# Kernel tuning notes

Hardware: AMD Instinct MI355X
Metric: run time of the kernel (lower is better)

Reference implementation:

```python
import math
import jax, jax.numpy as jnp
import numpy as np

B, S, H, NH = 4, 2048, 1024, 16
HD = H // NH  # 64


def _rope_cos_sin(seq_len, dim, base=10000.0):
    # freqs[j] = base^(-2j/dim), angles = outer(t, freqs)
    inv = 1.0 / (base ** (jnp.arange(0, dim, 2, dtype=jnp.float32) / dim))
    t = jnp.arange(seq_len, dtype=jnp.float32)
    ang = jnp.outer(t, inv)  # (S, dim//2)
    return jnp.cos(ang), jnp.sin(ang)


def _apply_rope(x, cos, sin):
    # x: (B, S, NH, HD); pairs are (x[2i], x[2i+1]) per torch view_as_complex on reshape(..., -1, 2)
    xr = x.reshape(*x.shape[:-1], HD // 2, 2)
    x0, x1 = xr[..., 0], xr[..., 1]
    c = cos[None, :, None, :]  # (1, S, 1, HD//2)
    s = sin[None, :, None, :]
    o0 = x0 * c - x1 * s
    o1 = x0 * s + x1 * c
    return jnp.stack([o0, o1], axis=-1).reshape(x.shape)


def setup_inputs() -> dict:
    key = jax.random.key(0)
    ks = jax.random.split(key, 5)
    scale = 1.0 / math.sqrt(H)
    return {
        "x": jax.random.normal(ks[0], (B, S, H), dtype=jnp.float32),
        "wq": jax.random.normal(ks[1], (H, H), dtype=jnp.float32) * scale,
        "wk": jax.random.normal(ks[2], (H, H), dtype=jnp.float32) * scale,
        "wv": jax.random.normal(ks[3], (H, H), dtype=jnp.float32) * scale,
        "wo": jax.random.normal(ks[4], (H, H), dtype=jnp.float32) * scale,
        "attention_mask": jnp.ones((B, S), dtype=jnp.int32),
    }


def reference(x, wq, wk, wv, wo, attention_mask):
    # Linear(bias=False): y = x @ W.T with W shape (out, in)
    q = jnp.einsum('bsh,oh->bso', x, wq).reshape(B, S, NH, HD)
    k = jnp.einsum('bsh,oh->bso', x, wk).reshape(B, S, NH, HD)
    v = jnp.einsum('bsh,oh->bso', x, wv).reshape(B, S, NH, HD)
    cos, sin = _rope_cos_sin(S, HD)
    q = _apply_rope(q, cos, sin)
    k = _apply_rope(k, cos, sin)
    # scores: (B, NH, S, S)
    scores = jnp.einsum('bqhd,bkhd->bhqk', q, k) / math.sqrt(HD)
    mask = attention_mask[:, None, None, :]  # (B,1,1,S)
    scores = jnp.where(mask == 0, -jnp.inf, scores)
    attn = jax.nn.softmax(scores, axis=-1)
    # attn_dropout: eval mode / p=0 -> identity
    out = jnp.einsum('bhqk,bkhd->bqhd', attn, v).reshape(B, S, H)
    return jnp.einsum('bsh,oh->bso', out, wo)
```

## Files before the change

kernel.cpp:

```cpp
#include <hip/hip_runtime.h>
#include <hip/hip_bf16.h>

#define B_   4
#define S_   2048
#define H_   1024
#define NH_  16
#define HD_  64
#define M_   8192
#define K_   1024

using bf16x8 = __bf16 __attribute__((ext_vector_type(8)));
using f32x4  = float __attribute__((ext_vector_type(4)));
using f32x16 = float __attribute__((ext_vector_type(16)));

__device__ inline f32x4 mfma16(bf16x8 a, bf16x8 b, f32x4 c) {
    return __builtin_amdgcn_mfma_f32_16x16x32_bf16(a, b, c, 0, 0, 0);
}
__device__ inline f32x16 mfma32(bf16x8 a, bf16x8 b, f32x16 c) {
    return __builtin_amdgcn_mfma_f32_32x32x16_bf16(a, b, c, 0, 0, 0);
}

__device__ inline unsigned short f2bf(float f) {
    __hip_bfloat16 h = __float2bfloat16(f);
    return *reinterpret_cast<unsigned short*>(&h);
}

__device__ inline unsigned cvt_pk_bf16(float lo, float hi) {
    unsigned r;
    asm("v_cvt_pk_bf16_f32 %0, %1, %2" : "=v"(r) : "v"(lo), "v"(hi));
    return r;
}

__device__ inline void perm32swap(unsigned &a, unsigned &b) {
    asm("v_permlane32_swap_b32 %0, %1" : "+v"(a), "+v"(b));
}

__device__ inline void gload_lds16(const unsigned short* g, unsigned short* l) {
    __builtin_amdgcn_global_load_lds(
        (const __attribute__((address_space(1))) void*)g,
        (__attribute__((address_space(3))) void*)l, 16, 0, 0);
}

#define EXP2F(x) __builtin_amdgcn_exp2f(x)


__global__ __launch_bounds__(256) void prep_convert(
    const float* __restrict__ x,  const float* __restrict__ wq,
    const float* __restrict__ wk, const float* __restrict__ wv,
    const float* __restrict__ wo, unsigned short* __restrict__ ws)
{
    size_t u = (size_t)blockIdx.x * 256 + threadIdx.x;
    const float* src; unsigned short* dst; size_t off;
    if (u < 2097152)      { src = x;  dst = ws;            off = u * 4; }
    else if (u < 2359296) { src = wq; dst = ws + 8388608;  off = (u - 2097152) * 4; }
    else if (u < 2621440) { src = wk; dst = ws + 9437184;  off = (u - 2359296) * 4; }
    else if (u < 2883584) { src = wv; dst = ws + 10485760; off = (u - 2621440) * 4; }
    else                  { src = wo; dst = ws + 11534336; off = (u - 2883584) * 4; }
    float4 v = *reinterpret_cast<const float4*>(src + off);
    ushort4 o;
    o.x = f2bf(v.x); o.y = f2bf(v.y); o.z = f2bf(v.z); o.w = f2bf(v.w);
    *reinterpret_cast<ushort4*>(dst + off) = o;
}

__global__ __launch_bounds__(256) void rope_table(
    float2* __restrict__ ropeb, const int* __restrict__ mask,
    float* __restrict__ biasb, int* __restrict__ kflagb)
{
    int idx = blockIdx.x * 256 + threadIdx.x;
    int pos = idx >> 5, i = idx & 31;
    float inv = expf(-(float)(2 * i) * (9.210340371976184f / 64.0f));
    float ang = (float)pos * inv;
    float2 cs; cs.x = cosf(ang); cs.y = sinf(ang);
    ropeb[idx] = cs;
    if (idx < B_ * S_)
        biasb[idx] = mask[idx] ? 0.0f : -__builtin_inff();
    if (idx < B_ * 32) {
        int b = idx >> 5, kt = idx & 31;
        int all = 1;
        for (int j = 0; j < 64; j++)
            all &= (mask[b * S_ + kt * 64 + j] != 0) ? 1 : 0;
        kflagb[idx] = all;
    }
}

template<int MODE>
__global__ __launch_bounds__(256, 2) void gemm_main(
    const unsigned short* __restrict__ A,
    const unsigned short* __restrict__ W,
    unsigned short* __restrict__ qbuf, unsigned short* __restrict__ kbuf,
    unsigned short* __restrict__ vtb, float* __restrict__ fout,
    const float* __restrict__ ropeb)
{
    __shared__ alignas(16) unsigned short Al[2][128 * 64];
    __shared__ alignas(16) unsigned short Bl[2][128 * 64];

    const int t = threadIdx.x;
    const int l = t & 63;
    const int w = t >> 6;
    const int lane_r = l & 15, lane_g = l >> 4;
    const int bn = blockIdx.x, bm = blockIdx.y;
    const size_t rowbase = (size_t)bm * 128;
    const int colbase = bn * 128;
    const int wm = (w >> 1) * 64, wn = (w & 1) * 64;
    const int which = (MODE == 0) ? (colbase >> 10) : 3;
    const float scale = (which == 0) ? 0.18033688089184827f : 1.0f;

    const int glrow  = l >> 3;
    const int glslot = (l & 7) ^ glrow;
    const unsigned short* ga = A + (rowbase + w * 8 + glrow) * K_ + glslot * 8;
    const unsigned short* gb = W + (size_t)(colbase + w * 8 + glrow) * K_ + glslot * 8;

#define GLA(bi, kt, i) gload_lds16(ga + (size_t)(i) * 32 * K_ + (kt) * 64, \
                                   &Al[bi][((i) * 32 + w * 8) * 64]);
#define GLB(bi, kt, i) gload_lds16(gb + (size_t)(i) * 32 * K_ + (kt) * 64, \
                                   &Bl[bi][((i) * 32 + w * 8) * 64]);
#define RDA(mt, kk) { int rowa = wm + (mt) * 16 + lane_r;                      \
    af[mt][kk] = *reinterpret_cast<const bf16x8*>((const char*)Al[cur] +       \
        ((rowa * 128 + (kk) * 64 + lane_g * 16) ^ ((rowa & 7) << 4))); }
#define RDB(nt, kk) { int rowb = wn + (nt) * 16 + lane_r;                      \
    bfr[nt][kk] = *reinterpret_cast<const bf16x8*>((const char*)Bl[cur] +      \
        ((rowb * 128 + (kk) * 64 + lane_g * 16) ^ ((rowb & 7) << 4))); }
#define MM(mb, nb)                                                             \
    if (MODE == 0 && which <= 1) {                                             \
        _Pragma("unroll")                                                      \
        for (int a = (nb); a < (nb) + 2; a++)                                  \
            _Pragma("unroll")                                                  \
            for (int b2 = (mb); b2 < (mb) + 2; b2++) {                         \
                acc[a][b2] = mfma16(bfr[a][0], af[b2][0], acc[a][b2]);         \
                acc[a][b2] = mfma16(bfr[a][1], af[b2][1], acc[a][b2]);         \
            }                                                                  \
    } else {                                                                   \
        _Pragma("unroll")                                                      \
        for (int mt = (mb); mt < (mb) + 2; mt++)                               \
            _Pragma("unroll")                                                  \
            for (int nt = (nb); nt < (nb) + 2; nt++) {                         \
                acc[mt][nt] = mfma16(af[mt][0], bfr[nt][0], acc[mt][nt]);      \
                acc[mt][nt] = mfma16(af[mt][1], bfr[nt][1], acc[mt][nt]);      \
            }                                                                  \
    }
#define BARS __builtin_amdgcn_s_barrier();                                     \
             asm volatile("s_waitcnt lgkmcnt(0)" ::: "memory");                \
             __builtin_amdgcn_s_setprio(1);
#define BARE __builtin_amdgcn_s_setprio(0); __builtin_amdgcn_s_barrier();

    f32x4 zero4 = {0.f, 0.f, 0.f, 0.f};
    f32x4 acc[4][4];
#pragma unroll
    for (int a = 0; a < 4; a++)
#pragma unroll
        for (int b2 = 0; b2 < 4; b2++) acc[a][b2] = zero4;

    GLA(0, 0, 0) GLA(0, 0, 1) GLA(0, 0, 2) GLA(0, 0, 3)
    GLB(0, 0, 0) GLB(0, 0, 1) GLB(0, 0, 2) GLB(0, 0, 3)
    __syncthreads();

    for (int kt = 0; kt < 16; kt++) {
        const int cur = kt & 1, nxt = cur ^ 1;
        const bool pf = (kt < 15);
        bf16x8 af[4][2], bfr[4][2];
        RDA(0, 0) RDA(0, 1) RDA(1, 0) RDA(1, 1)
        RDB(0, 0) RDB(0, 1) RDB(1, 0) RDB(1, 1)
        if (pf) { GLA(nxt, kt + 1, 0) GLA(nxt, kt + 1, 1) GLA(nxt, kt + 1, 2) }
        BARS MM(0, 0) BARE
        RDB(2, 0) RDB(2, 1) RDB(3, 0) RDB(3, 1)
        if (pf) { GLA(nxt, kt + 1, 3) GLB(nxt, kt + 1, 0) GLB(nxt, kt + 1, 1) }
        BARS MM(0, 2) BARE
        RDA(2, 0) RDA(2, 1) RDA(3, 0) RDA(3, 1)
        if (pf) { GLB(nxt, kt + 1, 2) GLB(nxt, kt + 1, 3) }
        BARS MM(2, 2) BARE
        __builtin_amdgcn_s_setprio(1);
        MM(2, 0)
        __builtin_amdgcn_s_setprio(0);
        asm volatile("s_waitcnt vmcnt(0)" ::: "memory");
        __builtin_amdgcn_s_barrier();
    }
#undef GLA
#undef GLB
#undef RDA
#undef RDB
#undef MM
#undef BARS
#undef BARE

    if (MODE == 1) {
        float* out = fout;
#pragma unroll
        for (int mt = 0; mt < 4; mt++)
#pragma unroll
            for (int nt = 0; nt < 4; nt++)
#pragma unroll
                for (int i = 0; i < 4; i++) {
                    size_t r = rowbase + wm + mt * 16 + lane_g * 4 + i;
                    int n = colbase + wn + nt * 16 + lane_r;
                    out[r * 1024 + n] = acc[mt][nt][i];
                }
    } else if (which <= 1) {
        unsigned short* out = which ? kbuf : qbuf;
#pragma unroll
        for (int a = 0; a < 4; a++) {
            int nbase = (colbase & 1023) + wn + a * 16 + 4 * lane_g;
            int h = nbase >> 6, d0 = nbase & 63;
#pragma unroll
            for (int b2 = 0; b2 < 4; b2++) {
                size_t r = rowbase + wm + b2 * 16 + lane_r;
                int bb  = (int)(r >> 11);
                int pos = (int)(r & 2047);
                float4 cs = *reinterpret_cast<const float4*>(
                    ropeb + pos * 64 + d0);
                float a0 = acc[a][b2][0], a1 = acc[a][b2][1];
                float a2 = acc[a][b2][2], a3 = acc[a][b2][3];
                float o0 = (a0 * cs.x - a1 * cs.y) * scale;
                float o1 = (a0 * cs.y + a1 * cs.x) * scale;
                float o2 = (a2 * cs.z - a3 * cs.w) * scale;
                float o3 = (a2 * cs.w + a3 * cs.z) * scale;
                uint2 o;
                o.x = cvt_pk_bf16(o0, o1);
                o.y = cvt_pk_bf16(o2, o3);
                *reinterpret_cast<uint2*>(
                    out + (((size_t)(bb * NH_ + h)) * S_ + pos) * 64 + d0) = o;
            }
        }
    } else {
#pragma unroll
        for (int a = 0; a < 4; a++)
#pragma unroll
            for (int b2 = 0; b2 < 4; b2++) {
                size_t rr = rowbase + wm + a * 16 + lane_g * 4;
                int n = (colbase & 1023) + wn + b2 * 16 + lane_r;
                int bb  = (int)(rr >> 11);
                int pos = (int)(rr & 2047);
                int h = n >> 6, d = n & 63;
                ushort4 o;
                o.x = f2bf(acc[a][b2][0]); o.y = f2bf(acc[a][b2][1]);
                o.z = f2bf(acc[a][b2][2]); o.w = f2bf(acc[a][b2][3]);
                *reinterpret_cast<ushort4*>(
                    vtb + (((size_t)(bb * NH_ + h)) * 64 + d) * S_ + pos) = o;
            }
    }
}

__global__ __launch_bounds__(256, 2) void attn_fwd(
    const unsigned short* __restrict__ qb, const unsigned short* __restrict__ kb,
    const unsigned short* __restrict__ vt, const float* __restrict__ biasb,
    const int* __restrict__ kflagb, unsigned short* __restrict__ ao)
{
    __shared__ alignas(16) unsigned short Kl[2][64 * 64];
    __shared__ alignas(16) unsigned short Vl[2][64 * 64];

    const int bid = blockIdx.x;
    const int xcd = bid & 7, idx = bid >> 3;
    const int bh = xcd * 8 + (idx >> 3);
    const int qt = idx & 7;
    const int b = bh >> 4, h = bh & 15;

    const int t = threadIdx.x, l = t & 63, w = t >> 6;
    const int lr = l & 31;
    const int hi = l >> 5;
    const int row8 = lr & 7;

    const unsigned short* qp = qb + (size_t)bh * S_ * 64;
    const unsigned short* kp = kb + (size_t)bh * S_ * 64;
    const unsigned short* vp = vt + (size_t)bh * 64 * S_;
    const float* bp = biasb + (size_t)b * S_;
    const int* kfl = kflagb + b * 32;

    bf16x8 qf[2][4];
#pragma unroll
    for (int qbk = 0; qbk < 2; qbk++) {
        int qrow = qt * 256 + w * 64 + qbk * 32 + lr;
#pragma unroll
        for (int ks = 0; ks < 4; ks++)
            qf[qbk][ks] = *reinterpret_cast<const bf16x8*>(
                qp + (size_t)qrow * 64 + ks * 16 + hi * 8);
    }

    f32x16 zero16;
#pragma unroll
    for (int r = 0; r < 16; r++) zero16[r] = 0.f;

    f32x16 oacc[2][2];
#pragma unroll
    for (int qbk = 0; qbk < 2; qbk++)
#pragma unroll
        for (int r = 0; r < 16; r++) { oacc[qbk][0][r] = 0.f; oacc[qbk][1][r] = 0.f; }
    float lsum[2] = {0.f, 0.f};

    const int grr = l >> 3;
    const int gss = ((l & 7) ^ grr) * 8;

#define STAGE(bi, kt)                                                          \
    {                                                                          \
        _Pragma("unroll")                                                      \
        for (int c = 0; c < 2; c++) {                                          \
            int rbase = w * 16 + c * 8;                                        \
            gload_lds16(kp + (size_t)((kt) * 64 + rbase + grr) * 64 + gss,     \
                        &Kl[bi][rbase * 64]);                                  \
            gload_lds16(vp + (size_t)(rbase + grr) * S_ + (kt) * 64 + gss,     \
                        &Vl[bi][rbase * 64]);                                  \
        }                                                                      \
    }

#define QKBLOCK(C0, C1)                                                        \
    {                                                                          \
        __builtin_amdgcn_s_setprio(1);                                         \
        _Pragma("unroll")                                                      \
        for (int T = 0; T < 2; T++) {                                          \
            int rowb = (32 * T + lr) * 128;                                    \
            bf16x8 kf0 = *reinterpret_cast<const bf16x8*>(                     \
                (const char*)Kl[cur] + rowb + ((hi ^ row8) << 4));             \
            sacc[0][T] = mfma32(kf0, qf[0][0], T ? (C1) : (C0));               \
            sacc[1][T] = mfma32(kf0, qf[1][0], T ? (C1) : (C0));               \
            _Pragma("unroll")                                                  \
            for (int ks = 1; ks < 4; ks++) {                                   \
                bf16x8 kfk = *reinterpret_cast<const bf16x8*>(                 \
                    (const char*)Kl[cur] + rowb + (((2 * ks + hi) ^ row8) << 4)); \
                sacc[0][T] = mfma32(kfk, qf[0][ks], sacc[0][T]);               \
                sacc[1][T] = mfma32(kfk, qf[1][ks], sacc[1][T]);               \
            }                                                                  \
        }                                                                      \
        __builtin_amdgcn_s_setprio(0);                                         \
    }

    STAGE(0, 0)

    for (int kt = 0; kt < 32; kt++) {
        const int cur = kt & 1;
        __syncthreads();
        if (kt < 31) STAGE(cur ^ 1, kt + 1)

        f32x16 sacc[2][2];
        if (kfl[kt]) {
            QKBLOCK(zero16, zero16)
        } else {
            f32x16 binit[2];
#pragma unroll
            for (int T = 0; T < 2; T++)
#pragma unroll
                for (int g = 0; g < 4; g++) {
                    float4 bv = *reinterpret_cast<const float4*>(
                        bp + kt * 64 + T * 32 + g * 8 + hi * 4);
                    binit[T][g * 4 + 0] = bv.x; binit[T][g * 4 + 1] = bv.y;
                    binit[T][g * 4 + 2] = bv.z; binit[T][g * 4 + 3] = bv.w;
                }
            QKBLOCK(binit[0], binit[1])
        }

        bf16x8 pa[2][4];
#pragma unroll
        for (int qbk = 0; qbk < 2; qbk++) {
            unsigned u[2][8];
            float r0 = 0.f, r1 = 0.f, r2 = 0.f, r3 = 0.f;
#pragma unroll
            for (int T = 0; T < 2; T++) {
                float p[16];
#pragma unroll
                for (int r = 0; r < 16; r++) p[r] = EXP2F(sacc[qbk][T][r]);
#pragma unroll
                for (int r = 0; r < 16; r += 4) {
                    r0 += p[r]; r1 += p[r + 1]; r2 += p[r + 2]; r3 += p[r + 3];
                }
#pragma unroll
                for (int bq = 0; bq < 4; bq++) {
                    u[T][bq * 2 + 0] = cvt_pk_bf16(p[bq * 4 + 0], p[bq * 4 + 1]);
                    u[T][bq * 2 + 1] = cvt_pk_bf16(p[bq * 4 + 2], p[bq * 4 + 3]);
                }
            }
            lsum[qbk] += (r0 + r1) + (r2 + r3);
#pragma unroll
            for (int ks = 0; ks < 4; ks++) {
                int T = ks >> 1, e = ks & 1;
                unsigned a0 = u[T][4 * e + 0], b0 = u[T][4 * e + 2];
                unsigned a1 = u[T][4 * e + 1], b1 = u[T][4 * e + 3];
                perm32swap(a0, b0);
                perm32swap(a1, b1);
                unsigned q4[4] = {a0, a1, b0, b1};
                pa[qbk][ks] = *reinterpret_cast<const bf16x8*>(q4);
            }
        }

        __builtin_amdgcn_s_setprio(1);
#pragma unroll
        for (int dt = 0; dt < 2; dt++) {
            int rowb = (32 * dt + lr) * 128;
#pragma unroll
            for (int ks = 0; ks < 4; ks++) {
                bf16x8 vf = *reinterpret_cast<const bf16x8*>(
                    (const char*)Vl[cur] + rowb + (((2 * ks + hi) ^ row8) << 4));
                oacc[0][dt] = mfma32(vf, pa[0][ks], oacc[0][dt]);
                oacc[1][dt] = mfma32(vf, pa[1][ks], oacc[1][dt]);
            }
        }
        __builtin_amdgcn_s_setprio(0);
    }
#undef STAGE
#undef QKBLOCK

#pragma unroll
    for (int qbk = 0; qbk < 2; qbk++) {
        float ls = lsum[qbk];
        ls += __shfl_xor(ls, 32);
        float rl = 1.0f / ls;
        size_t obase = ((size_t)(b * S_) + qt * 256 + w * 64 + qbk * 32 + lr) * 1024 + h * 64;
#pragma unroll
        for (int dt = 0; dt < 2; dt++)
#pragma unroll
            for (int g = 0; g < 4; g++) {
                uint2 o;
                o.x = cvt_pk_bf16(oacc[qbk][dt][g * 4 + 0] * rl, oacc[qbk][dt][g * 4 + 1] * rl);
                o.y = cvt_pk_bf16(oacc[qbk][dt][g * 4 + 2] * rl, oacc[qbk][dt][g * 4 + 3] * rl);
                *reinterpret_cast<uint2*>(ao + obase + 32 * dt + 8 * g + 4 * hi) = o;
            }
    }
}

extern "C" void kernel_launch(void* const* d_in, const int* in_sizes, int n_in,
                              void* d_out, int out_size, void* d_ws, size_t ws_size,
                              hipStream_t stream)
{
    const float* x  = (const float*)d_in[0];
    const float* wq = (const float*)d_in[1];
    const float* wk = (const float*)d_in[2];
    const float* wv = (const float*)d_in[3];
    const float* wo = (const float*)d_in[4];
    const int* mask = (const int*)d_in[5];

    unsigned short* ws   = (unsigned short*)d_ws;
    unsigned short* xb   = ws;
    unsigned short* wqkv = ws + 8388608;
    unsigned short* wob  = ws + 11534336;
    unsigned short* qbuf = ws + 12582912;
    unsigned short* kbuf = ws + 20971520;
    unsigned short* vtb  = ws + 29360128;
    float* ropeb = (float*)(ws + 37748736);
    float* biasb = (float*)(ws + 38010880);
    int* kflagb  = (int*)(biasb + 8192);
    unsigned short* aob = xb;

    prep_convert<<<12288, 256, 0, stream>>>(x, wq, wk, wv, wo, ws);
    rope_table<<<256, 256, 0, stream>>>((float2*)ropeb, mask, biasb, kflagb);

    gemm_main<0><<<dim3(24, 64), 256, 0, stream>>>(
        xb, wqkv, qbuf, kbuf, vtb, nullptr, ropeb);

    attn_fwd<<<512, 256, 0, stream>>>(qbuf, kbuf, vtb, biasb, kflagb, aob);

    gemm_main<1><<<dim3(8, 64), 256, 0, stream>>>(
        aob, wob, nullptr, nullptr, nullptr, (float*)d_out, nullptr);
}
```

Measured before the change: 200.6 us.

## Fuse rope table into convert kernel and stage 128 keys per attention barrier

```diff
diff --git a/kernel.cpp b/kernel.cpp
--- a/kernel.cpp
+++ b/kernel.cpp
@@ -47,39 +47,38 @@
 __global__ __launch_bounds__(256) void prep_convert(
     const float* __restrict__ x,  const float* __restrict__ wq,
     const float* __restrict__ wk, const float* __restrict__ wv,
-    const float* __restrict__ wo, unsigned short* __restrict__ ws)
+    const float* __restrict__ wo, unsigned short* __restrict__ ws,
+    const int* __restrict__ mask, float2* __restrict__ ropeb,
+    float* __restrict__ biasb, int* __restrict__ kflagb)
 {
     size_t u = (size_t)blockIdx.x * 256 + threadIdx.x;
-    const float* src; unsigned short* dst; size_t off;
-    if (u < 2097152)      { src = x;  dst = ws;            off = u * 4; }
-    else if (u < 2359296) { src = wq; dst = ws + 8388608;  off = (u - 2097152) * 4; }
-    else if (u < 2621440) { src = wk; dst = ws + 9437184;  off = (u - 2359296) * 4; }
-    else if (u < 2883584) { src = wv; dst = ws + 10485760; off = (u - 2621440) * 4; }
-    else                  { src = wo; dst = ws + 11534336; off = (u - 2883584) * 4; }
-    float4 v = *reinterpret_cast<const float4*>(src + off);
-    ushort4 o;
-    o.x = f2bf(v.x); o.y = f2bf(v.y); o.z = f2bf(v.z); o.w = f2bf(v.w);
-    *reinterpret_cast<ushort4*>(dst + off) = o;
-}
-
-__global__ __launch_bounds__(256) void rope_table(
-    float2* __restrict__ ropeb, const int* __restrict__ mask,
-    float* __restrict__ biasb, int* __restrict__ kflagb)
-{
-    int idx = blockIdx.x * 256 + threadIdx.x;
-    int pos = idx >> 5, i = idx & 31;
-    float inv = expf(-(float)(2 * i) * (9.210340371976184f / 64.0f));
-    float ang = (float)pos * inv;
-    float2 cs; cs.x = cosf(ang); cs.y = sinf(ang);
-    ropeb[idx] = cs;
-    if (idx < B_ * S_)
-        biasb[idx] = mask[idx] ? 0.0f : -__builtin_inff();
-    if (idx < B_ * 32) {
-        int b = idx >> 5, kt = idx & 31;
-        int all = 1;
-        for (int j = 0; j < 64; j++)
-            all &= (mask[b * S_ + kt * 64 + j] != 0) ? 1 : 0;
-        kflagb[idx] = all;
+    if (u < 3145728) {
+        const float* src; unsigned short* dst; size_t off;
+        if (u < 2097152)      { src = x;  dst = ws;            off = u * 4; }
+        else if (u < 2359296) { src = wq; dst = ws + 8388608;  off = (u - 2097152) * 4; }
+        else if (u < 2621440) { src = wk; dst = ws + 9437184;  off = (u - 2359296) * 4; }
+        else if (u < 2883584) { src = wv; dst = ws + 10485760; off = (u - 2621440) * 4; }
+        else                  { src = wo; dst = ws + 11534336; off = (u - 2883584) * 4; }
+        float4 v = *reinterpret_cast<const float4*>(src + off);
+        ushort4 o;
+        o.x = f2bf(v.x); o.y = f2bf(v.y); o.z = f2bf(v.z); o.w = f2bf(v.w);
+        *reinterpret_cast<ushort4*>(dst + off) = o;
+    } else {
+        int idx = (int)(u - 3145728);
+        int pos = idx >> 5, i = idx & 31;
+        float inv = expf(-(float)(2 * i) * (9.210340371976184f / 64.0f));
+        float ang = (float)pos * inv;
+        float2 cs; cs.x = cosf(ang); cs.y = sinf(ang);
+        ropeb[idx] = cs;
+        if (idx < B_ * S_)
+            biasb[idx] = mask[idx] ? 0.0f : -__builtin_inff();
+        if (idx < B_ * 32) {
+            int b = idx >> 5, kt = idx & 31;
+            int all = 1;
+            for (int j = 0; j < 64; j++)
+                all &= (mask[b * S_ + kt * 64 + j] != 0) ? 1 : 0;
+            kflagb[idx] = all;
+        }
     }
 }
 
@@ -244,8 +243,8 @@
     const unsigned short* __restrict__ vt, const float* __restrict__ biasb,
     const int* __restrict__ kflagb, unsigned short* __restrict__ ao)
 {
-    __shared__ alignas(16) unsigned short Kl[2][64 * 64];
-    __shared__ alignas(16) unsigned short Vl[2][64 * 64];
+    __shared__ alignas(16) unsigned short Kl[2][2][64 * 64];
+    __shared__ alignas(16) unsigned short Vl[2][2][64 * 64];
 
     const int bid = blockIdx.x;
     const int xcd = bid & 7, idx = bid >> 3;
@@ -288,32 +287,35 @@
     const int grr = l >> 3;
     const int gss = ((l & 7) ^ grr) * 8;
 
-#define STAGE(bi, kt)                                                          \
+#define STAGE(bi, mt)                                                          \
     {                                                                          \
         _Pragma("unroll")                                                      \
-        for (int c = 0; c < 2; c++) {                                          \
-            int rbase = w * 16 + c * 8;                                        \
-            gload_lds16(kp + (size_t)((kt) * 64 + rbase + grr) * 64 + gss,     \
-                        &Kl[bi][rbase * 64]);                                  \
-            gload_lds16(vp + (size_t)(rbase + grr) * S_ + (kt) * 64 + gss,     \
-                        &Vl[bi][rbase * 64]);                                  \
+        for (int sub = 0; sub < 2; sub++) {                                    \
+            _Pragma("unroll")                                                  \
+            for (int c = 0; c < 2; c++) {                                      \
+                int rbase = w * 16 + c * 8;                                    \
+                gload_lds16(kp + (size_t)((mt) * 128 + sub * 64 + rbase + grr) * 64 + gss, \
+                            &Kl[bi][sub][rbase * 64]);                         \
+                gload_lds16(vp + (size_t)(rbase + grr) * S_ + (mt) * 128 + sub * 64 + gss, \
+                            &Vl[bi][sub][rbase * 64]);                         \
+            }                                                                  \
         }                                                                      \
     }
 
-#define QKBLOCK(C0, C1)                                                        \
+#define QKBLOCK(KLP, C0, C1)                                                   \
     {                                                                          \
         __builtin_amdgcn_s_setprio(1);                                         \
         _Pragma("unroll")                                                      \
         for (int T = 0; T < 2; T++) {                                          \
             int rowb = (32 * T + lr) * 128;                                    \
             bf16x8 kf0 = *reinterpret_cast<const bf16x8*>(                     \
-                (const char*)Kl[cur] + rowb + ((hi ^ row8) << 4));             \
+                (const char*)(KLP) + rowb + ((hi ^ row8) << 4));               \
             sacc[0][T] = mfma32(kf0, qf[0][0], T ? (C1) : (C0));               \
             sacc[1][T] = mfma32(kf0, qf[1][0], T ? (C1) : (C0));               \
             _Pragma("unroll")                                                  \
             for (int ks = 1; ks < 4; ks++) {                                   \
                 bf16x8 kfk = *reinterpret_cast<const bf16x8*>(                 \
-                    (const char*)Kl[cur] + rowb + (((2 * ks + hi) ^ row8) << 4)); \
+                    (const char*)(KLP) + rowb + (((2 * ks + hi) ^ row8) << 4)); \
                 sacc[0][T] = mfma32(kfk, qf[0][ks], sacc[0][T]);               \
                 sacc[1][T] = mfma32(kfk, qf[1][ks], sacc[1][T]);               \
             }                                                                  \
@@ -323,74 +325,78 @@
 
     STAGE(0, 0)
 
-    for (int kt = 0; kt < 32; kt++) {
-        const int cur = kt & 1;
+    for (int mt = 0; mt < 16; mt++) {
+        const int cur = mt & 1;
         __syncthreads();
-        if (kt < 31) STAGE(cur ^ 1, kt + 1)
-
-        f32x16 sacc[2][2];
-        if (kfl[kt]) {
-            QKBLOCK(zero16, zero16)
-        } else {
-            f32x16 binit[2];
-#pragma unroll
-            for (int T = 0; T < 2; T++)
-#pragma unroll
-                for (int g = 0; g < 4; g++) {
-                    float4 bv = *reinterpret_cast<const float4*>(
-                        bp + kt * 64 + T * 32 + g * 8 + hi * 4);
-                    binit[T][g * 4 + 0] = bv.x; binit[T][g * 4 + 1] = bv.y;
-                    binit[T][g * 4 + 2] = bv.z; binit[T][g * 4 + 3] = bv.w;
+        if (mt < 15) STAGE(cur ^ 1, mt + 1)
+
+#pragma unroll
+        for (int sub = 0; sub < 2; sub++) {
+            const int kt64 = mt * 2 + sub;
+            f32x16 sacc[2][2];
+            if (kfl[kt64]) {
+                QKBLOCK(Kl[cur][sub], zero16, zero16)
+            } else {
+                f32x16 binit[2];
+#pragma unroll
+                for (int T = 0; T < 2; T++)
+#pragma unroll
+                    for (int g = 0; g < 4; g++) {
+                        float4 bv = *reinterpret_cast<const float4*>(
+                            bp + kt64 * 64 + T * 32 + g * 8 + hi * 4);
+                        binit[T][g * 4 + 0] = bv.x; binit[T][g * 4 + 1] = bv.y;
+                        binit[T][g * 4 + 2] = bv.z; binit[T][g * 4 + 3] = bv.w;
+                    }
+                QKBLOCK(Kl[cur][sub], binit[0], binit[1])
+            }
+
+            bf16x8 pa[2][4];
+#pragma unroll
+            for (int qbk = 0; qbk < 2; qbk++) {
+                unsigned u[2][8];
+                float r0 = 0.f, r1 = 0.f, r2 = 0.f, r3 = 0.f;
+#pragma unroll
+                for (int T = 0; T < 2; T++) {
+                    float p[16];
+#pragma unroll
+                    for (int r = 0; r < 16; r++) p[r] = EXP2F(sacc[qbk][T][r]);
+#pragma unroll
+                    for (int r = 0; r < 16; r += 4) {
+                        r0 += p[r]; r1 += p[r + 1]; r2 += p[r + 2]; r3 += p[r + 3];
+                    }
+#pragma unroll
+                    for (int bq = 0; bq < 4; bq++) {
+                        u[T][bq * 2 + 0] = cvt_pk_bf16(p[bq * 4 + 0], p[bq * 4 + 1]);
+                        u[T][bq * 2 + 1] = cvt_pk_bf16(p[bq * 4 + 2], p[bq * 4 + 3]);
+                    }
                 }
-            QKBLOCK(binit[0], binit[1])
+                lsum[qbk] += (r0 + r1) + (r2 + r3);
+#pragma unroll
+                for (int ks = 0; ks < 4; ks++) {
+                    int T = ks >> 1, e = ks & 1;
+                    unsigned a0 = u[T][4 * e + 0], b0 = u[T][4 * e + 2];
+                    unsigned a1 = u[T][4 * e + 1], b1 = u[T][4 * e + 3];
+                    perm32swap(a0, b0);
+                    perm32swap(a1, b1);
+                    unsigned q4[4] = {a0, a1, b0, b1};
+                    pa[qbk][ks] = *reinterpret_cast<const bf16x8*>(q4);
+                }
+            }
+
+            __builtin_amdgcn_s_setprio(1);
+#pragma unroll
+            for (int dt = 0; dt < 2; dt++) {
+                int rowb = (32 * dt + lr) * 128;
+#pragma unroll
+                for (int ks = 0; ks < 4; ks++) {
+                    bf16x8 vf = *reinterpret_cast<const bf16x8*>(
+                        (const char*)Vl[cur][sub] + rowb + (((2 * ks + hi) ^ row8) << 4));
+                    oacc[0][dt] = mfma32(vf, pa[0][ks], oacc[0][dt]);
+                    oacc[1][dt] = mfma32(vf, pa[1][ks], oacc[1][dt]);
+                }
+            }
+            __builtin_amdgcn_s_setprio(0);
         }
-
-        bf16x8 pa[2][4];
-#pragma unroll
-        for (int qbk = 0; qbk < 2; qbk++) {
-            unsigned u[2][8];
-            float r0 = 0.f, r1 = 0.f, r2 = 0.f, r3 = 0.f;
-#pragma unroll
-            for (int T = 0; T < 2; T++) {
-                float p[16];
-#pragma unroll
-                for (int r = 0; r < 16; r++) p[r] = EXP2F(sacc[qbk][T][r]);
-#pragma unroll
-                for (int r = 0; r < 16; r += 4) {
-                    r0 += p[r]; r1 += p[r + 1]; r2 += p[r + 2]; r3 += p[r + 3];
-                }
-#pragma unroll
-                for (int bq = 0; bq < 4; bq++) {
-                    u[T][bq * 2 + 0] = cvt_pk_bf16(p[bq * 4 + 0], p[bq * 4 + 1]);
-                    u[T][bq * 2 + 1] = cvt_pk_bf16(p[bq * 4 + 2], p[bq * 4 + 3]);
-                }
-            }
-            lsum[qbk] += (r0 + r1) + (r2 + r3);
-#pragma unroll
-            for (int ks = 0; ks < 4; ks++) {
-                int T = ks >> 1, e = ks & 1;
-                unsigned a0 = u[T][4 * e + 0], b0 = u[T][4 * e + 2];
-                unsigned a1 = u[T][4 * e + 1], b1 = u[T][4 * e + 3];
-                perm32swap(a0, b0);
-                perm32swap(a1, b1);
-                unsigned q4[4] = {a0, a1, b0, b1};
-                pa[qbk][ks] = *reinterpret_cast<const bf16x8*>(q4);
-            }
-        }
-
-        __builtin_amdgcn_s_setprio(1);
-#pragma unroll
-        for (int dt = 0; dt < 2; dt++) {
-            int rowb = (32 * dt + lr) * 128;
-#pragma unroll
-            for (int ks = 0; ks < 4; ks++) {
-                bf16x8 vf = *reinterpret_cast<const bf16x8*>(
-                    (const char*)Vl[cur] + rowb + (((2 * ks + hi) ^ row8) << 4));
-                oacc[0][dt] = mfma32(vf, pa[0][ks], oacc[0][dt]);
-                oacc[1][dt] = mfma32(vf, pa[1][ks], oacc[1][dt]);
-            }
-        }
-        __builtin_amdgcn_s_setprio(0);
     }
 #undef STAGE
 #undef QKBLOCK
@@ -436,8 +442,8 @@
     int* kflagb  = (int*)(biasb + 8192);
     unsigned short* aob = xb;
 
-    prep_convert<<<12288, 256, 0, stream>>>(x, wq, wk, wv, wo, ws);
-    rope_table<<<256, 256, 0, stream>>>((float2*)ropeb, mask, biasb, kflagb);
+    prep_convert<<<12544, 256, 0, stream>>>(
+        x, wq, wk, wv, wo, ws, mask, (float2*)ropeb, biasb, kflagb);
 
     gemm_main<0><<<dim3(24, 64), 256, 0, stream>>>(
         xb, wqkv, qbuf, kbuf, vtb, nullptr, ropeb);
```

Result: slower. 206.0 us (+2.7%).
